# Performance work log

Hardware: AMD Instinct MI355X
Metric: run time of the kernel (lower is better)

The kernel has to match this reference:

```python
import jax, jax.numpy as jnp
import numpy as np

N_NODES = 500000
N_EDGES = 4000000
IN_DIM = 2
HID = 8
N_ITERS = 3


def _edge_net(x, row, col, e1_w, e1_b, e2_w, e2_b):
    # bi = x[col], bo = x[row]; B = cat([bi, bo]) is detached in torch
    B = jax.lax.stop_gradient(jnp.concatenate([x[col], x[row]], axis=-1))  # [E, 2*F]
    h = jnp.tanh(B @ e1_w + e1_b)
    return jax.nn.sigmoid(h @ e2_w + e2_b)  # [E, 1]


def _node_net(x, row, col, edge_attr, n1_w, n1_b, n2_w, n2_b):
    e = jax.lax.stop_gradient(edge_attr)  # [E, 1], detached in torch
    bi = x[col] * e  # [E, F]
    bo = x[row] * e
    mi = jax.ops.segment_sum(bo, col, num_segments=N_NODES)  # scatter_add over col
    mo = jax.ops.segment_sum(bi, row, num_segments=N_NODES)  # scatter_add over row
    M = jax.lax.stop_gradient(jnp.concatenate([mi, mo, x], axis=-1))  # [N, 3*F]
    h = jnp.tanh(M @ n1_w + n1_b)
    return jnp.tanh(h @ n2_w + n2_b)  # [N, HID]


def setup_inputs() -> dict:
    key = jax.random.key(0)
    ks = jax.random.split(key, 12)
    F = IN_DIM + HID  # 10
    s = lambda fan_in: 1.0 / np.sqrt(fan_in)
    return {
        "x": jax.random.normal(ks[0], (N_NODES, IN_DIM), jnp.float32),
        "edge_index": jax.random.randint(ks[1], (2, N_EDGES), 0, N_NODES),
        "win_w": jax.random.uniform(ks[2], (IN_DIM, HID), jnp.float32, -s(IN_DIM), s(IN_DIM)),
        "win_b": jax.random.uniform(ks[3], (HID,), jnp.float32, -s(IN_DIM), s(IN_DIM)),
        "e1_w": jax.random.uniform(ks[4], (2 * F, HID), jnp.float32, -s(2 * F), s(2 * F)),
        "e1_b": jax.random.uniform(ks[5], (HID,), jnp.float32, -s(2 * F), s(2 * F)),
        "e2_w": jax.random.uniform(ks[6], (HID, 1), jnp.float32, -s(HID), s(HID)),
        "e2_b": jax.random.uniform(ks[7], (1,), jnp.float32, -s(HID), s(HID)),
        "n1_w": jax.random.uniform(ks[8], (3 * F, HID), jnp.float32, -s(3 * F), s(3 * F)),
        "n1_b": jax.random.uniform(ks[9], (HID,), jnp.float32, -s(3 * F), s(3 * F)),
        "n2_w": jax.random.uniform(ks[10], (HID, HID), jnp.float32, -s(HID), s(HID)),
        "n2_b": jax.random.uniform(ks[11], (HID,), jnp.float32, -s(HID), s(HID)),
    }


def reference(x, edge_index, win_w, win_b, e1_w, e1_b, e2_w, e2_b, n1_w, n1_b, n2_w, n2_b):
    row, col = edge_index[0], edge_index[1]
    X = x
    H = jnp.tanh(X @ win_w + win_b)  # input_network
    xcat = jnp.concatenate([H, X], axis=-1)  # [N, 10]
    for _ in range(N_ITERS):
        e = _edge_net(xcat, row, col, e1_w, e1_b, e2_w, e2_b)
        H = _node_net(xcat, row, col, e, n1_w, n1_b, n2_w, n2_b)
        xcat = jnp.concatenate([H, X], axis=-1)
    out = _edge_net(xcat, row, col, e1_w, e1_b, e2_w, e2_b)
    return out.squeeze(-1)  # [E]
```

## Files before the change

### kernel.cpp

```cpp
#include <hip/hip_runtime.h>
#include <hip/hip_fp16.h>
#include <math.h>

#define N_NODES 500000
#define N_EDGES 4000000
#define FDIM 10
#define HID 8

#define DSPACE (2 * N_NODES)
#define NB 512
#define BSHIFT 11
#define BMASK 2047
#define NB_USED ((DSPACE + BMASK) / 2048)

#define IN_BLOCKS ((N_NODES + 255) / 256)
#define ROWS_PAD (IN_BLOCKS * 256)
#define NODE_BLOCKS2 ((N_NODES + 127) / 128)

__device__ __forceinline__ float fast_tanh(float x) {
    float e = __builtin_amdgcn_exp2f(x * 2.885390082f);
    return 1.0f - 2.0f * __builtin_amdgcn_rcpf(e + 1.0f);
}
__device__ __forceinline__ float fast_sigmoid(float x) {
    float e = __builtin_amdgcn_exp2f(-1.442695041f * x);
    return __builtin_amdgcn_rcpf(1.0f + e);
}

__device__ __forceinline__ float2 h2f2(float bits) {
    union { float f; __half2 h; } u; u.f = bits;
    return __half22float2(u.h);
}
__device__ __forceinline__ float f2h2(float a, float b) {
    union { float f; __half2 h; } u; u.h = __floats2half2_rn(a, b);
    return u.f;
}

__device__ __forceinline__ void unpack10(float4 H, float X, float* o) {
    float2 p0 = h2f2(H.x), p1 = h2f2(H.y), p2 = h2f2(H.z), p3 = h2f2(H.w), p4 = h2f2(X);
    o[0] = p0.x; o[1] = p0.y; o[2] = p1.x; o[3] = p1.y; o[4] = p2.x;
    o[5] = p2.y; o[6] = p3.x; o[7] = p3.y; o[8] = p4.x; o[9] = p4.y;
}

__device__ __forceinline__ void fma8(float* a, float xk, float4 wa, float4 wb) {
    a[0] += xk * wa.x; a[1] += xk * wa.y; a[2] += xk * wa.z; a[3] += xk * wa.w;
    a[4] += xk * wb.x; a[5] += xk * wb.y; a[6] += xk * wb.z; a[7] += xk * wb.w;
}

__global__ __launch_bounds__(256) void input_kernel(const float* __restrict__ x,
                                                    const float* __restrict__ win_w,
                                                    const float* __restrict__ win_b,
                                                    float4* __restrict__ xh,
                                                    float* __restrict__ xs) {
    int n = blockIdx.x * 256 + threadIdx.x;
    float x0 = 0.f, x1 = 0.f;
    if (n < N_NODES) { x0 = x[2 * n]; x1 = x[2 * n + 1]; }
    float h[HID];
#pragma unroll
    for (int j = 0; j < HID; j++)
        h[j] = fast_tanh(x0 * win_w[j] + x1 * win_w[HID + j] + win_b[j]);
    xh[n] = make_float4(f2h2(h[0], h[1]), f2h2(h[2], h[3]),
                        f2h2(h[4], h[5]), f2h2(h[6], h[7]));
    xs[n] = f2h2(x0, x1);
}

__global__ void bucket_hist_kernel(const int* __restrict__ row,
                                   const int* __restrict__ col,
                                   int* __restrict__ g_cnt) {
    __shared__ int s_cnt[NB];
    int tid = threadIdx.x;
    for (int i = tid; i < NB; i += 256) s_cnt[i] = 0;
    __syncthreads();
    int base = blockIdx.x * 4096;
#pragma unroll
    for (int k = 0; k < 16; k++) {
        int e = base + k * 256 + tid;
        if (e < N_EDGES) {
            int c = col[e], r = row[e];
            atomicAdd(&s_cnt[(2 * c) >> BSHIFT], 1);
            atomicAdd(&s_cnt[(2 * r + 1) >> BSHIFT], 1);
        }
    }
    __syncthreads();
    for (int i = tid; i < NB; i += 256) {
        int v = s_cnt[i];
        if (v) atomicAdd(&g_cnt[i], v);
    }
}

__global__ void bucket_scan_kernel(const int* __restrict__ g_cnt,
                                   int* __restrict__ bucket_base,
                                   int* __restrict__ bucket_cur) {
    __shared__ int s[NB];
    int t = threadIdx.x;
    int c = g_cnt[t];
    s[t] = c;
    __syncthreads();
    for (int off = 1; off < NB; off <<= 1) {
        int v = (t >= off) ? s[t - off] : 0;
        __syncthreads();
        s[t] += v;
        __syncthreads();
    }
    int ex = s[t] - c;
    bucket_base[t] = ex;
    bucket_cur[t] = ex;
    if (t == NB - 1) bucket_base[NB] = s[t];
}

__global__ void bin_kernel(const int* __restrict__ row,
                           const int* __restrict__ col,
                           int* __restrict__ bucket_cur,
                           unsigned int* __restrict__ binned) {
    __shared__ int s_cnt[NB];
    __shared__ int s_start[NB];
    __shared__ int s_cur[NB];
    __shared__ int s_gbase[NB];
    __shared__ unsigned int s_items[8192];
    __shared__ unsigned short s_ibkt[8192];

    int tid = threadIdx.x;
    if (tid < NB) s_cnt[tid] = 0;
    __syncthreads();

    int base = blockIdx.x * 4096;
    int cc[4], rr[4];
#pragma unroll
    for (int k = 0; k < 4; k++) {
        int e = base + k * 1024 + tid;
        bool ok = (e < N_EDGES);
        cc[k] = ok ? col[e] : -1;
        rr[k] = ok ? row[e] : -1;
        if (ok) {
            atomicAdd(&s_cnt[(2 * cc[k]) >> BSHIFT], 1);
            atomicAdd(&s_cnt[(2 * rr[k] + 1) >> BSHIFT], 1);
        }
    }
    __syncthreads();

    if (tid < NB) s_start[tid] = s_cnt[tid];
    __syncthreads();
    for (int off = 1; off < NB; off <<= 1) {
        int v = 0;
        if (tid < NB && tid >= off) v = s_start[tid - off];
        __syncthreads();
        if (tid < NB) s_start[tid] += v;
        __syncthreads();
    }
    if (tid < NB) {
        int ex = s_start[tid] - s_cnt[tid];
        s_start[tid] = ex;
        s_cur[tid] = ex;
    }
    __syncthreads();

#pragma unroll
    for (int k = 0; k < 4; k++) {
        if (cc[k] >= 0) {
            int d0 = 2 * cc[k];
            int b0 = d0 >> BSHIFT;
            int s0 = atomicAdd(&s_cur[b0], 1);
            s_items[s0] = ((unsigned)(d0 & BMASK) << 19) | (unsigned)rr[k];
            s_ibkt[s0] = (unsigned short)b0;
            int d1 = 2 * rr[k] + 1;
            int b1 = d1 >> BSHIFT;
            int s1 = atomicAdd(&s_cur[b1], 1);
            s_items[s1] = ((unsigned)(d1 & BMASK) << 19) | (unsigned)cc[k];
            s_ibkt[s1] = (unsigned short)b1;
        }
    }
    __syncthreads();

    if (tid < NB) s_gbase[tid] = atomicAdd(&bucket_cur[tid], s_cnt[tid]);
    __syncthreads();

    int tot = s_start[NB - 1] + s_cnt[NB - 1];
    for (int s = tid; s < tot; s += 1024) {
        int b = s_ibkt[s];
        int g = s_gbase[b] + (s - s_start[b]);
        binned[g] = s_items[s];
    }
}

__global__ void csr_kernel(const unsigned int* __restrict__ binned,
                           const int* __restrict__ bucket_base,
                           int* __restrict__ offs,
                           int* __restrict__ entries) {
    __shared__ int s_deg[2048];
    __shared__ int s_cur[2048];
    __shared__ int s_pair[1024];

    int t = threadIdx.x;
    int b = blockIdx.x;
    if (b == 0 && t == 0) offs[DSPACE] = 2 * N_EDGES;

    int ebase = bucket_base[b];
    int eend = bucket_base[b + 1];

    s_deg[t] = 0;
    s_deg[t + 1024] = 0;
    __syncthreads();

    for (int p = ebase + t; p < eend; p += 1024)
        atomicAdd(&s_deg[binned[p] >> 19], 1);
    __syncthreads();

    int d0 = s_deg[2 * t], d1 = s_deg[2 * t + 1];
    s_pair[t] = d0 + d1;
    __syncthreads();
    for (int off = 1; off < 1024; off <<= 1) {
        int v = (t >= off) ? s_pair[t - off] : 0;
        __syncthreads();
        s_pair[t] += v;
        __syncthreads();
    }
    int pex = s_pair[t] - (d0 + d1);
    s_cur[2 * t] = pex;
    s_cur[2 * t + 1] = pex + d0;

    int dest0 = b * 2048 + 2 * t;
    if (dest0 < DSPACE) offs[dest0] = ebase + pex;
    if (dest0 + 1 < DSPACE) offs[dest0 + 1] = ebase + pex + d0;
    __syncthreads();

    for (int p = ebase + t; p < eend; p += 1024) {
        unsigned int it = binned[p];
        int dl = it >> 19;
        int other = it & 0x7FFFF;
        int pos = atomicAdd(&s_cur[dl], 1);
        entries[ebase + pos] = other;
    }
}

__global__ __launch_bounds__(256) void edge_kernel(const int* __restrict__ row,
                                                   const int* __restrict__ col,
                                                   const float4* __restrict__ xh,
                                                   const float* __restrict__ xs,
                                                   const float* __restrict__ e1_w,
                                                   const float* __restrict__ e1_b,
                                                   const float* __restrict__ e2_w,
                                                   const float* __restrict__ e2_b,
                                                   float* __restrict__ out) {
    __shared__ float4 s_w4[40];
    __shared__ float s_b[HID];
    __shared__ float s_v[HID];
    __shared__ float s_c[1];
    int tid = threadIdx.x;
    float* wf = (float*)s_w4;
    if (tid < 160) wf[tid] = e1_w[tid];
    else if (tid < 168) s_b[tid - 160] = e1_b[tid - 160];
    else if (tid < 176) s_v[tid - 168] = e2_w[tid - 168];
    else if (tid == 176) s_c[0] = e2_b[0];
    __syncthreads();

    int i = blockIdx.x * 256 + tid;
    if (i >= N_EDGES) return;

    int r = row[i], c = col[i];
    float4 aH = xh[c]; float aX = xs[c];
    float4 bH = xh[r]; float bX = xs[r];
    float a[FDIM], bb[FDIM];
    unpack10(aH, aX, a);
    unpack10(bH, bX, bb);

    float acc[HID];
#pragma unroll
    for (int j = 0; j < HID; j++) acc[j] = s_b[j];
#pragma unroll
    for (int k = 0; k < FDIM; k++)
        fma8(acc, a[k], s_w4[2 * k], s_w4[2 * k + 1]);
#pragma unroll
    for (int k = 0; k < FDIM; k++)
        fma8(acc, bb[k], s_w4[20 + 2 * k], s_w4[21 + 2 * k]);

    float d = s_c[0];
#pragma unroll
    for (int j = 0; j < HID; j++) d += fast_tanh(acc[j]) * s_v[j];
    out[i] = fast_sigmoid(d);
}

__global__ __launch_bounds__(256) void node_kernel(const float4* __restrict__ xh,
                                                   const float* __restrict__ xs,
                                                   const int* __restrict__ offs,
                                                   const int* __restrict__ entries,
                                                   const float* __restrict__ e1_w,
                                                   const float* __restrict__ e1_b,
                                                   const float* __restrict__ e2_w,
                                                   const float* __restrict__ e2_b,
                                                   const float* __restrict__ n1_w,
                                                   const float* __restrict__ n1_b,
                                                   const float* __restrict__ n2_w,
                                                   const float* __restrict__ n2_b,
                                                   float4* __restrict__ xh_next) {
    __shared__ float4 s_e1w4[40];
    __shared__ float s_e1b[HID];
    __shared__ float s_e2w[HID];
    __shared__ float s_e2b[1];
    __shared__ float4 s_n1w4[60];
    __shared__ float s_n1b[HID];
    __shared__ float4 s_n2w4[16];
    __shared__ float s_n2b[HID];
    __shared__ float s_mo[128 * 11];

    int tid = threadIdx.x;
    float* e1f = (float*)s_e1w4;
    if (tid < 160) e1f[tid] = e1_w[tid];
    else if (tid < 168) s_e1b[tid - 160] = e1_b[tid - 160];
    else if (tid < 176) s_e2w[tid - 168] = e2_w[tid - 168];
    else if (tid == 176) s_e2b[0] = e2_b[0];
    float* n1f = (float*)s_n1w4;
    if (tid < 240) n1f[tid] = n1_w[tid];
    else if (tid < 248) s_n1b[tid - 240] = n1_b[tid - 240];
    float* n2f = (float*)s_n2w4;
    if (tid < 64) n2f[tid] = n2_w[tid];
    else if (tid < 72) s_n2b[tid - 64] = n2_b[tid - 64];
    __syncthreads();

    bool up = tid >= 128;
    int lt = up ? tid - 128 : tid;
    int n = blockIdx.x * 128 + lt;
    bool act = n < N_NODES;

    int selfBase = up ? 20 : 0;
    int othBase  = up ? 0 : 20;
    int dest = 2 * n + (up ? 1 : 0);

    float e2w_r[HID];
#pragma unroll
    for (int j = 0; j < HID; j++) e2w_r[j] = s_e2w[j];
    float e2b_r = s_e2b[0];

    float xn[FDIM];
    float m[FDIM];
#pragma unroll
    for (int k = 0; k < FDIM; k++) m[k] = 0.f;

    if (act) {
        float4 hN = xh[n]; float xN = xs[n];
        unpack10(hN, xN, xn);

        float us[HID];
#pragma unroll
        for (int j = 0; j < HID; j++) us[j] = s_e1b[j];
#pragma unroll
        for (int k = 0; k < FDIM; k++)
            fma8(us, xn[k], s_e1w4[selfBase + 2 * k], s_e1w4[selfBase + 2 * k + 1]);

        int p0 = offs[dest], p1 = offs[dest + 1];
        float4 cH = make_float4(0.f, 0.f, 0.f, 0.f); float cX = 0.f;
        if (p0 < p1) { int o = entries[p0]; cH = xh[o]; cX = xs[o]; }
        for (int p = p0; p < p1; ++p) {
            float4 nH = cH; float nX = cX;
            if (p + 1 < p1) { int o2 = entries[p + 1]; nH = xh[o2]; nX = xs[o2]; }

            float xo[FDIM];
            unpack10(cH, cX, xo);

            float acc[HID];
#pragma unroll
            for (int j = 0; j < HID; j++) acc[j] = us[j];
#pragma unroll
            for (int k = 0; k < FDIM; k++)
                fma8(acc, xo[k], s_e1w4[othBase + 2 * k], s_e1w4[othBase + 2 * k + 1]);

            float d = e2b_r;
#pragma unroll
            for (int j = 0; j < HID; j++) d += fast_tanh(acc[j]) * e2w_r[j];
            float e = fast_sigmoid(d);
#pragma unroll
            for (int k = 0; k < FDIM; k++) m[k] += e * xo[k];

            cH = nH; cX = nX;
        }
    }

    if (up && act) {
        int lb = lt * 11;
#pragma unroll
        for (int k = 0; k < FDIM; k++) s_mo[lb + k] = m[k];
    }
    __syncthreads();

    if (!up && act) {
        int lb = lt * 11;
        float h1[HID];
#pragma unroll
        for (int j = 0; j < HID; j++) h1[j] = s_n1b[j];
#pragma unroll
        for (int k = 0; k < FDIM; k++)
            fma8(h1, m[k], s_n1w4[2 * k], s_n1w4[2 * k + 1]);
#pragma unroll
        for (int k = 0; k < FDIM; k++)
            fma8(h1, s_mo[lb + k], s_n1w4[20 + 2 * k], s_n1w4[21 + 2 * k]);
#pragma unroll
        for (int k = 0; k < FDIM; k++)
            fma8(h1, xn[k], s_n1w4[40 + 2 * k], s_n1w4[41 + 2 * k]);
#pragma unroll
        for (int j = 0; j < HID; j++) h1[j] = fast_tanh(h1[j]);

        float H[HID];
#pragma unroll
        for (int j = 0; j < HID; j++) H[j] = s_n2b[j];
#pragma unroll
        for (int k = 0; k < HID; k++)
            fma8(H, h1[k], s_n2w4[2 * k], s_n2w4[2 * k + 1]);
#pragma unroll
        for (int j = 0; j < HID; j++) H[j] = fast_tanh(H[j]);

        xh_next[n] = make_float4(f2h2(H[0], H[1]), f2h2(H[2], H[3]),
                                 f2h2(H[4], H[5]), f2h2(H[6], H[7]));
    }
}

extern "C" void kernel_launch(void* const* d_in, const int* in_sizes, int n_in,
                              void* d_out, int out_size, void* d_ws, size_t ws_size,
                              hipStream_t stream) {
    const float* x      = (const float*)d_in[0];
    const int*   eidx   = (const int*)d_in[1];
    const float* win_w  = (const float*)d_in[2];
    const float* win_b  = (const float*)d_in[3];
    const float* e1_w   = (const float*)d_in[4];
    const float* e1_b   = (const float*)d_in[5];
    const float* e2_w   = (const float*)d_in[6];
    const float* e2_b   = (const float*)d_in[7];
    const float* n1_w   = (const float*)d_in[8];
    const float* n1_b   = (const float*)d_in[9];
    const float* n2_w   = (const float*)d_in[10];
    const float* n2_b   = (const float*)d_in[11];
    float* out = (float*)d_out;

    const int* row = eidx;
    const int* col = eidx + N_EDGES;

    float4* xh0 = (float4*)d_ws;
    float4* xh1 = xh0 + ROWS_PAD;
    float*  xs  = (float*)(xh1 + ROWS_PAD);
    unsigned int* binned = (unsigned int*)(xs + ROWS_PAD);
    int* entries = (int*)(binned + 2 * (size_t)N_EDGES);
    int* offs        = entries + 2 * (size_t)N_EDGES;
    int* g_cnt       = offs + DSPACE + 64;
    int* bucket_base = g_cnt + NB;
    int* bucket_cur  = bucket_base + NB + 64;

    const int BLK = 256;
    int edge_blocks = (N_EDGES + BLK - 1) / BLK;
    int chunk_blocks = (N_EDGES + 4095) / 4096;

    hipMemsetAsync(g_cnt, 0, NB * sizeof(int), stream);
    bucket_hist_kernel<<<chunk_blocks, 256, 0, stream>>>(row, col, g_cnt);
    bucket_scan_kernel<<<1, NB, 0, stream>>>(g_cnt, bucket_base, bucket_cur);
    bin_kernel<<<chunk_blocks, 1024, 0, stream>>>(row, col, bucket_cur, binned);
    csr_kernel<<<NB_USED, 1024, 0, stream>>>(binned, bucket_base, offs, entries);

    input_kernel<<<IN_BLOCKS, BLK, 0, stream>>>(x, win_w, win_b, xh0, xs);

    float4* cur = xh0;
    float4* nxt = xh1;
    for (int it = 0; it < 3; it++) {
        node_kernel<<<NODE_BLOCKS2, BLK, 0, stream>>>(
            cur, xs, offs, entries, e1_w, e1_b, e2_w, e2_b,
            n1_w, n1_b, n2_w, n2_b, nxt);
        float4* t = cur; cur = nxt; nxt = t;
    }

    edge_kernel<<<edge_blocks, BLK, 0, stream>>>(
        row, col, cur, xs, e1_w, e1_b, e2_w, e2_b, out);
}
```

Baseline: 930.9 us.

## Split node kernel into per-side gather and node-net kernels using fp16 dot2

```diff
diff --git a/kernel.cpp b/kernel.cpp
--- a/kernel.cpp
+++ b/kernel.cpp
@@ -15,7 +15,22 @@
 
 #define IN_BLOCKS ((N_NODES + 255) / 256)
 #define ROWS_PAD (IN_BLOCKS * 256)
-#define NODE_BLOCKS2 ((N_NODES + 127) / 128)
+#define MSTRIDE ((size_t)ROWS_PAD * 10)
+
+typedef _Float16 h2v __attribute__((ext_vector_type(2)));
+
+__device__ __forceinline__ h2v u2h(unsigned x) {
+    union { unsigned u; h2v h; } t; t.u = x; return t.h;
+}
+__device__ __forceinline__ unsigned packh2(float a, float b) {
+    union { __half2 h; unsigned u; } t; t.h = __floats2half2_rn(a, b); return t.u;
+}
+__device__ __forceinline__ float rfl_f(float x) {
+    return __int_as_float(__builtin_amdgcn_readfirstlane(__float_as_int(x)));
+}
+__device__ __forceinline__ unsigned rfl_u(unsigned x) {
+    return (unsigned)__builtin_amdgcn_readfirstlane((int)x);
+}
 
 __device__ __forceinline__ float fast_tanh(float x) {
     float e = __builtin_amdgcn_exp2f(x * 2.885390082f);
@@ -26,31 +41,11 @@
     return __builtin_amdgcn_rcpf(1.0f + e);
 }
 
-__device__ __forceinline__ float2 h2f2(float bits) {
-    union { float f; __half2 h; } u; u.f = bits;
-    return __half22float2(u.h);
-}
-__device__ __forceinline__ float f2h2(float a, float b) {
-    union { float f; __half2 h; } u; u.h = __floats2half2_rn(a, b);
-    return u.f;
-}
-
-__device__ __forceinline__ void unpack10(float4 H, float X, float* o) {
-    float2 p0 = h2f2(H.x), p1 = h2f2(H.y), p2 = h2f2(H.z), p3 = h2f2(H.w), p4 = h2f2(X);
-    o[0] = p0.x; o[1] = p0.y; o[2] = p1.x; o[3] = p1.y; o[4] = p2.x;
-    o[5] = p2.y; o[6] = p3.x; o[7] = p3.y; o[8] = p4.x; o[9] = p4.y;
-}
-
-__device__ __forceinline__ void fma8(float* a, float xk, float4 wa, float4 wb) {
-    a[0] += xk * wa.x; a[1] += xk * wa.y; a[2] += xk * wa.z; a[3] += xk * wa.w;
-    a[4] += xk * wb.x; a[5] += xk * wb.y; a[6] += xk * wb.z; a[7] += xk * wb.w;
-}
-
 __global__ __launch_bounds__(256) void input_kernel(const float* __restrict__ x,
                                                     const float* __restrict__ win_w,
                                                     const float* __restrict__ win_b,
-                                                    float4* __restrict__ xh,
-                                                    float* __restrict__ xs) {
+                                                    uint4* __restrict__ xh,
+                                                    unsigned* __restrict__ xs) {
     int n = blockIdx.x * 256 + threadIdx.x;
     float x0 = 0.f, x1 = 0.f;
     if (n < N_NODES) { x0 = x[2 * n]; x1 = x[2 * n + 1]; }
@@ -58,9 +53,9 @@
 #pragma unroll
     for (int j = 0; j < HID; j++)
         h[j] = fast_tanh(x0 * win_w[j] + x1 * win_w[HID + j] + win_b[j]);
-    xh[n] = make_float4(f2h2(h[0], h[1]), f2h2(h[2], h[3]),
-                        f2h2(h[4], h[5]), f2h2(h[6], h[7]));
-    xs[n] = f2h2(x0, x1);
+    xh[n] = make_uint4(packh2(h[0], h[1]), packh2(h[2], h[3]),
+                       packh2(h[4], h[5]), packh2(h[6], h[7]));
+    xs[n] = packh2(x0, x1);
 }
 
 __global__ void bucket_hist_kernel(const int* __restrict__ row,
@@ -231,184 +226,251 @@
     }
 }
 
+__global__ __launch_bounds__(256, 6) void node_loop_kernel(
+        const uint4* __restrict__ xh,
+        const unsigned* __restrict__ xs,
+        const int* __restrict__ offs,
+        const int* __restrict__ entries,
+        const float* __restrict__ e1_w,
+        const float* __restrict__ e1_b,
+        const float* __restrict__ e2_w,
+        const float* __restrict__ e2_b,
+        float* __restrict__ m_out) {
+    __shared__ uint4 s_self4[10];
+    __shared__ unsigned s_oth[40];
+    __shared__ float s_scal[17];
+
+    int tid = threadIdx.x;
+    int side = (blockIdx.x >= IN_BLOCKS) ? 1 : 0;
+    int selfBase = side ? 10 : 0;
+    int othBase  = side ? 0 : 10;
+
+    unsigned* s_self = (unsigned*)s_self4;
+    if (tid < 40) {
+        int kk = tid >> 3, j = tid & 7;
+        s_self[tid] = packh2(e1_w[(selfBase + 2 * kk) * HID + j],
+                             e1_w[(selfBase + 2 * kk + 1) * HID + j]);
+        s_oth[tid]  = packh2(e1_w[(othBase + 2 * kk) * HID + j],
+                             e1_w[(othBase + 2 * kk + 1) * HID + j]);
+    } else if (tid < 48) s_scal[tid - 40] = e1_b[tid - 48 + 8];
+    else if (tid < 56) s_scal[tid - 40] = e2_w[tid - 48];
+    else if (tid == 56) s_scal[16] = e2_b[0];
+    __syncthreads();
+
+    unsigned so[40];
+#pragma unroll
+    for (int i = 0; i < 40; i++) so[i] = rfl_u(s_oth[i]);
+    float sb[HID], sv[HID];
+#pragma unroll
+    for (int j = 0; j < HID; j++) { sb[j] = rfl_f(s_scal[j]); sv[j] = rfl_f(s_scal[8 + j]); }
+    float sc = rfl_f(s_scal[16]);
+
+    int n = (blockIdx.x - side * IN_BLOCKS) * 256 + tid;
+    if (n >= N_NODES) return;
+    int dest = 2 * n + side;
+
+    uint4 xq = xh[n]; unsigned xx = xs[n];
+    unsigned xp[5] = { xq.x, xq.y, xq.z, xq.w, xx };
+    float us[HID];
+#pragma unroll
+    for (int j = 0; j < HID; j++) us[j] = sb[j];
+#pragma unroll
+    for (int kk = 0; kk < 5; kk++) {
+        uint4 wa = s_self4[2 * kk];
+        uint4 wb = s_self4[2 * kk + 1];
+        h2v a = u2h(xp[kk]);
+        us[0] = __builtin_amdgcn_fdot2(a, u2h(wa.x), us[0], false);
+        us[1] = __builtin_amdgcn_fdot2(a, u2h(wa.y), us[1], false);
+        us[2] = __builtin_amdgcn_fdot2(a, u2h(wa.z), us[2], false);
+        us[3] = __builtin_amdgcn_fdot2(a, u2h(wa.w), us[3], false);
+        us[4] = __builtin_amdgcn_fdot2(a, u2h(wb.x), us[4], false);
+        us[5] = __builtin_amdgcn_fdot2(a, u2h(wb.y), us[5], false);
+        us[6] = __builtin_amdgcn_fdot2(a, u2h(wb.z), us[6], false);
+        us[7] = __builtin_amdgcn_fdot2(a, u2h(wb.w), us[7], false);
+    }
+
+    int p0 = offs[dest], p1 = offs[dest + 1];
+    float m[FDIM];
+#pragma unroll
+    for (int k = 0; k < FDIM; k++) m[k] = 0.f;
+
+    uint4 cH = make_uint4(0, 0, 0, 0); unsigned cX = 0;
+    if (p0 < p1) { int o = entries[p0]; cH = xh[o]; cX = xs[o]; }
+    for (int p = p0; p < p1; ++p) {
+        uint4 nH = cH; unsigned nX = cX;
+        if (p + 1 < p1) { int o2 = entries[p + 1]; nH = xh[o2]; nX = xs[o2]; }
+
+        unsigned cp[5] = { cH.x, cH.y, cH.z, cH.w, cX };
+        float acc[HID];
+#pragma unroll
+        for (int j = 0; j < HID; j++) acc[j] = us[j];
+#pragma unroll
+        for (int kk = 0; kk < 5; kk++) {
+            h2v a = u2h(cp[kk]);
+#pragma unroll
+            for (int j = 0; j < HID; j++)
+                acc[j] = __builtin_amdgcn_fdot2(a, u2h(so[kk * 8 + j]), acc[j], false);
+        }
+        float d = sc;
+#pragma unroll
+        for (int j = 0; j < HID; j++) d += fast_tanh(acc[j]) * sv[j];
+        float e = fast_sigmoid(d);
+#pragma unroll
+        for (int kk = 0; kk < 5; kk++) {
+            h2v a = u2h(cp[kk]);
+            m[2 * kk]     += e * (float)a.x;
+            m[2 * kk + 1] += e * (float)a.y;
+        }
+        cH = nH; cX = nX;
+    }
+
+    float2* md = (float2*)(m_out + (size_t)side * MSTRIDE + (size_t)n * 10);
+    md[0] = make_float2(m[0], m[1]);
+    md[1] = make_float2(m[2], m[3]);
+    md[2] = make_float2(m[4], m[5]);
+    md[3] = make_float2(m[6], m[7]);
+    md[4] = make_float2(m[8], m[9]);
+}
+
+__global__ __launch_bounds__(256) void node_net_kernel(
+        const uint4* __restrict__ xh,
+        const unsigned* __restrict__ xs,
+        const float* __restrict__ m_in,
+        const float* __restrict__ n1_w,
+        const float* __restrict__ n1_b,
+        const float* __restrict__ n2_w,
+        const float* __restrict__ n2_b,
+        uint4* __restrict__ xh_next) {
+    __shared__ float s_n1w[30 * HID];
+    __shared__ float s_n1b[HID];
+    __shared__ float s_n2w[HID * HID];
+    __shared__ float s_n2b[HID];
+    int tid = threadIdx.x;
+    if (tid < 240) s_n1w[tid] = n1_w[tid];
+    else if (tid < 248) s_n1b[tid - 240] = n1_b[tid - 240];
+    if (tid < 64) s_n2w[tid] = n2_w[tid];
+    else if (tid < 72) s_n2b[tid - 64] = n2_b[tid - 64];
+    __syncthreads();
+
+    int n = blockIdx.x * 256 + tid;
+    if (n >= N_NODES) return;
+
+    float mi[FDIM], mo[FDIM];
+    const float2* p_mi = (const float2*)(m_in + (size_t)n * 10);
+    const float2* p_mo = (const float2*)(m_in + MSTRIDE + (size_t)n * 10);
+#pragma unroll
+    for (int k = 0; k < 5; k++) {
+        float2 a = p_mi[k]; mi[2 * k] = a.x; mi[2 * k + 1] = a.y;
+        float2 b = p_mo[k]; mo[2 * k] = b.x; mo[2 * k + 1] = b.y;
+    }
+    uint4 xq = xh[n]; unsigned xx = xs[n];
+    unsigned xp[5] = { xq.x, xq.y, xq.z, xq.w, xx };
+    float xn[FDIM];
+#pragma unroll
+    for (int kk = 0; kk < 5; kk++) {
+        h2v a = u2h(xp[kk]);
+        xn[2 * kk] = (float)a.x; xn[2 * kk + 1] = (float)a.y;
+    }
+
+    float h1[HID];
+#pragma unroll
+    for (int j = 0; j < HID; j++) h1[j] = s_n1b[j];
+#pragma unroll
+    for (int k = 0; k < FDIM; k++) {
+#pragma unroll
+        for (int j = 0; j < HID; j++) {
+            h1[j] += mi[k] * s_n1w[k * HID + j];
+            h1[j] += mo[k] * s_n1w[(FDIM + k) * HID + j];
+            h1[j] += xn[k] * s_n1w[(2 * FDIM + k) * HID + j];
+        }
+    }
+#pragma unroll
+    for (int j = 0; j < HID; j++) h1[j] = fast_tanh(h1[j]);
+
+    float H[HID];
+#pragma unroll
+    for (int j = 0; j < HID; j++) H[j] = s_n2b[j];
+#pragma unroll
+    for (int k = 0; k < HID; k++) {
+#pragma unroll
+        for (int j = 0; j < HID; j++) H[j] += h1[k] * s_n2w[k * HID + j];
+    }
+#pragma unroll
+    for (int j = 0; j < HID; j++) H[j] = fast_tanh(H[j]);
+
+    xh_next[n] = make_uint4(packh2(H[0], H[1]), packh2(H[2], H[3]),
+                            packh2(H[4], H[5]), packh2(H[6], H[7]));
+}
+
 __global__ __launch_bounds__(256) void edge_kernel(const int* __restrict__ row,
                                                    const int* __restrict__ col,
-                                                   const float4* __restrict__ xh,
-                                                   const float* __restrict__ xs,
+                                                   const uint4* __restrict__ xh,
+                                                   const unsigned* __restrict__ xs,
                                                    const float* __restrict__ e1_w,
                                                    const float* __restrict__ e1_b,
                                                    const float* __restrict__ e2_w,
                                                    const float* __restrict__ e2_b,
                                                    float* __restrict__ out) {
-    __shared__ float4 s_w4[40];
-    __shared__ float s_b[HID];
-    __shared__ float s_v[HID];
-    __shared__ float s_c[1];
+    __shared__ unsigned s_top[40];
+    __shared__ uint4 s_bot4[10];
+    __shared__ float s_scal[17];
     int tid = threadIdx.x;
-    float* wf = (float*)s_w4;
-    if (tid < 160) wf[tid] = e1_w[tid];
-    else if (tid < 168) s_b[tid - 160] = e1_b[tid - 160];
-    else if (tid < 176) s_v[tid - 168] = e2_w[tid - 168];
-    else if (tid == 176) s_c[0] = e2_b[0];
-    __syncthreads();
+    unsigned* s_bot = (unsigned*)s_bot4;
+    if (tid < 40) {
+        int kk = tid >> 3, j = tid & 7;
+        s_top[tid] = packh2(e1_w[(2 * kk) * HID + j], e1_w[(2 * kk + 1) * HID + j]);
+        s_bot[tid] = packh2(e1_w[(FDIM + 2 * kk) * HID + j], e1_w[(FDIM + 2 * kk + 1) * HID + j]);
+    } else if (tid < 48) s_scal[tid - 40] = e1_b[tid - 48 + 8];
+    else if (tid < 56) s_scal[tid - 40] = e2_w[tid - 48];
+    else if (tid == 56) s_scal[16] = e2_b[0];
+    __syncthreads();
+
+    unsigned st[40];
+#pragma unroll
+    for (int i = 0; i < 40; i++) st[i] = rfl_u(s_top[i]);
+    float sb[HID], sv[HID];
+#pragma unroll
+    for (int j = 0; j < HID; j++) { sb[j] = rfl_f(s_scal[j]); sv[j] = rfl_f(s_scal[8 + j]); }
+    float sc = rfl_f(s_scal[16]);
 
     int i = blockIdx.x * 256 + tid;
     if (i >= N_EDGES) return;
 
     int r = row[i], c = col[i];
-    float4 aH = xh[c]; float aX = xs[c];
-    float4 bH = xh[r]; float bX = xs[r];
-    float a[FDIM], bb[FDIM];
-    unpack10(aH, aX, a);
-    unpack10(bH, bX, bb);
+    uint4 aq = xh[c]; unsigned ax = xs[c];
+    uint4 bq = xh[r]; unsigned bx = xs[r];
+    unsigned ap[5] = { aq.x, aq.y, aq.z, aq.w, ax };
+    unsigned bp[5] = { bq.x, bq.y, bq.z, bq.w, bx };
 
     float acc[HID];
 #pragma unroll
-    for (int j = 0; j < HID; j++) acc[j] = s_b[j];
-#pragma unroll
-    for (int k = 0; k < FDIM; k++)
-        fma8(acc, a[k], s_w4[2 * k], s_w4[2 * k + 1]);
-#pragma unroll
-    for (int k = 0; k < FDIM; k++)
-        fma8(acc, bb[k], s_w4[20 + 2 * k], s_w4[21 + 2 * k]);
-
-    float d = s_c[0];
-#pragma unroll
-    for (int j = 0; j < HID; j++) d += fast_tanh(acc[j]) * s_v[j];
+    for (int j = 0; j < HID; j++) acc[j] = sb[j];
+#pragma unroll
+    for (int kk = 0; kk < 5; kk++) {
+        h2v a = u2h(ap[kk]);
+#pragma unroll
+        for (int j = 0; j < HID; j++)
+            acc[j] = __builtin_amdgcn_fdot2(a, u2h(st[kk * 8 + j]), acc[j], false);
+    }
+#pragma unroll
+    for (int kk = 0; kk < 5; kk++) {
+        uint4 wa = s_bot4[2 * kk];
+        uint4 wb = s_bot4[2 * kk + 1];
+        h2v b = u2h(bp[kk]);
+        acc[0] = __builtin_amdgcn_fdot2(b, u2h(wa.x), acc[0], false);
+        acc[1] = __builtin_amdgcn_fdot2(b, u2h(wa.y), acc[1], false);
+        acc[2] = __builtin_amdgcn_fdot2(b, u2h(wa.z), acc[2], false);
+        acc[3] = __builtin_amdgcn_fdot2(b, u2h(wa.w), acc[3], false);
+        acc[4] = __builtin_amdgcn_fdot2(b, u2h(wb.x), acc[4], false);
+        acc[5] = __builtin_amdgcn_fdot2(b, u2h(wb.y), acc[5], false);
+        acc[6] = __builtin_amdgcn_fdot2(b, u2h(wb.z), acc[6], false);
+        acc[7] = __builtin_amdgcn_fdot2(b, u2h(wb.w), acc[7], false);
+    }
+
+    float d = sc;
+#pragma unroll
+    for (int j = 0; j < HID; j++) d += fast_tanh(acc[j]) * sv[j];
     out[i] = fast_sigmoid(d);
-}
-
-__global__ __launch_bounds__(256) void node_kernel(const float4* __restrict__ xh,
-                                                   const float* __restrict__ xs,
-                                                   const int* __restrict__ offs,
-                                                   const int* __restrict__ entries,
-                                                   const float* __restrict__ e1_w,
-                                                   const float* __restrict__ e1_b,
-                                                   const float* __restrict__ e2_w,
-                                                   const float* __restrict__ e2_b,
-                                                   const float* __restrict__ n1_w,
-                                                   const float* __restrict__ n1_b,
-                                                   const float* __restrict__ n2_w,
-                                                   const float* __restrict__ n2_b,
-                                                   float4* __restrict__ xh_next) {
-    __shared__ float4 s_e1w4[40];
-    __shared__ float s_e1b[HID];
-    __shared__ float s_e2w[HID];
-    __shared__ float s_e2b[1];
-    __shared__ float4 s_n1w4[60];
-    __shared__ float s_n1b[HID];
-    __shared__ float4 s_n2w4[16];
-    __shared__ float s_n2b[HID];
-    __shared__ float s_mo[128 * 11];
-
-    int tid = threadIdx.x;
-    float* e1f = (float*)s_e1w4;
-    if (tid < 160) e1f[tid] = e1_w[tid];
-    else if (tid < 168) s_e1b[tid - 160] = e1_b[tid - 160];
-    else if (tid < 176) s_e2w[tid - 168] = e2_w[tid - 168];
-    else if (tid == 176) s_e2b[0] = e2_b[0];
-    float* n1f = (float*)s_n1w4;
-    if (tid < 240) n1f[tid] = n1_w[tid];
-    else if (tid < 248) s_n1b[tid - 240] = n1_b[tid - 240];
-    float* n2f = (float*)s_n2w4;
-    if (tid < 64) n2f[tid] = n2_w[tid];
-    else if (tid < 72) s_n2b[tid - 64] = n2_b[tid - 64];
-    __syncthreads();
-
-    bool up = tid >= 128;
-    int lt = up ? tid - 128 : tid;
-    int n = blockIdx.x * 128 + lt;
-    bool act = n < N_NODES;
-
-    int selfBase = up ? 20 : 0;
-    int othBase  = up ? 0 : 20;
-    int dest = 2 * n + (up ? 1 : 0);
-
-    float e2w_r[HID];
-#pragma unroll
-    for (int j = 0; j < HID; j++) e2w_r[j] = s_e2w[j];
-    float e2b_r = s_e2b[0];
-
-    float xn[FDIM];
-    float m[FDIM];
-#pragma unroll
-    for (int k = 0; k < FDIM; k++) m[k] = 0.f;
-
-    if (act) {
-        float4 hN = xh[n]; float xN = xs[n];
-        unpack10(hN, xN, xn);
-
-        float us[HID];
-#pragma unroll
-        for (int j = 0; j < HID; j++) us[j] = s_e1b[j];
-#pragma unroll
-        for (int k = 0; k < FDIM; k++)
-            fma8(us, xn[k], s_e1w4[selfBase + 2 * k], s_e1w4[selfBase + 2 * k + 1]);
-
-        int p0 = offs[dest], p1 = offs[dest + 1];
-        float4 cH = make_float4(0.f, 0.f, 0.f, 0.f); float cX = 0.f;
-        if (p0 < p1) { int o = entries[p0]; cH = xh[o]; cX = xs[o]; }
-        for (int p = p0; p < p1; ++p) {
-            float4 nH = cH; float nX = cX;
-            if (p + 1 < p1) { int o2 = entries[p + 1]; nH = xh[o2]; nX = xs[o2]; }
-
-            float xo[FDIM];
-            unpack10(cH, cX, xo);
-
-            float acc[HID];
-#pragma unroll
-            for (int j = 0; j < HID; j++) acc[j] = us[j];
-#pragma unroll
-            for (int k = 0; k < FDIM; k++)
-                fma8(acc, xo[k], s_e1w4[othBase + 2 * k], s_e1w4[othBase + 2 * k + 1]);
-
-            float d = e2b_r;
-#pragma unroll
-            for (int j = 0; j < HID; j++) d += fast_tanh(acc[j]) * e2w_r[j];
-            float e = fast_sigmoid(d);
-#pragma unroll
-            for (int k = 0; k < FDIM; k++) m[k] += e * xo[k];
-
-            cH = nH; cX = nX;
-        }
-    }
-
-    if (up && act) {
-        int lb = lt * 11;
-#pragma unroll
-        for (int k = 0; k < FDIM; k++) s_mo[lb + k] = m[k];
-    }
-    __syncthreads();
-
-    if (!up && act) {
-        int lb = lt * 11;
-        float h1[HID];
-#pragma unroll
-        for (int j = 0; j < HID; j++) h1[j] = s_n1b[j];
-#pragma unroll
-        for (int k = 0; k < FDIM; k++)
-            fma8(h1, m[k], s_n1w4[2 * k], s_n1w4[2 * k + 1]);
-#pragma unroll
-        for (int k = 0; k < FDIM; k++)
-            fma8(h1, s_mo[lb + k], s_n1w4[20 + 2 * k], s_n1w4[21 + 2 * k]);
-#pragma unroll
-        for (int k = 0; k < FDIM; k++)
-            fma8(h1, xn[k], s_n1w4[40 + 2 * k], s_n1w4[41 + 2 * k]);
-#pragma unroll
-        for (int j = 0; j < HID; j++) h1[j] = fast_tanh(h1[j]);
-
-        float H[HID];
-#pragma unroll
-        for (int j = 0; j < HID; j++) H[j] = s_n2b[j];
-#pragma unroll
-        for (int k = 0; k < HID; k++)
-            fma8(H, h1[k], s_n2w4[2 * k], s_n2w4[2 * k + 1]);
-#pragma unroll
-        for (int j = 0; j < HID; j++) H[j] = fast_tanh(H[j]);
-
-        xh_next[n] = make_float4(f2h2(H[0], H[1]), f2h2(H[2], H[3]),
-                                 f2h2(H[4], H[5]), f2h2(H[6], H[7]));
-    }
 }
 
 extern "C" void kernel_launch(void* const* d_in, const int* in_sizes, int n_in,
@@ -431,15 +493,18 @@
     const int* row = eidx;
     const int* col = eidx + N_EDGES;
 
-    float4* xh0 = (float4*)d_ws;
-    float4* xh1 = xh0 + ROWS_PAD;
-    float*  xs  = (float*)(xh1 + ROWS_PAD);
-    unsigned int* binned = (unsigned int*)(xs + ROWS_PAD);
-    int* entries = (int*)(binned + 2 * (size_t)N_EDGES);
-    int* offs        = entries + 2 * (size_t)N_EDGES;
-    int* g_cnt       = offs + DSPACE + 64;
-    int* bucket_base = g_cnt + NB;
-    int* bucket_cur  = bucket_base + NB + 64;
+    char* w = (char*)d_ws;
+    uint4* xh0 = (uint4*)w;            w += (size_t)ROWS_PAD * 16;
+    uint4* xh1 = (uint4*)w;            w += (size_t)ROWS_PAD * 16;
+    unsigned* xs = (unsigned*)w;       w += (size_t)ROWS_PAD * 4;
+    int* entries = (int*)w;            w += (size_t)2 * N_EDGES * 4;
+    int* offs = (int*)w;               w += (size_t)(DSPACE + 64) * 4;
+    int* g_cnt = (int*)w;              w += NB * 4;
+    int* bucket_base = (int*)w;        w += (NB + 64) * 4;
+    int* bucket_cur = (int*)w;         w += NB * 4;
+    w = (char*)(((uintptr_t)w + 255) & ~(uintptr_t)255);
+    float* m = (float*)w;
+    unsigned int* binned = (unsigned int*)w;
 
     const int BLK = 256;
     int edge_blocks = (N_EDGES + BLK - 1) / BLK;
@@ -453,13 +518,14 @@
 
     input_kernel<<<IN_BLOCKS, BLK, 0, stream>>>(x, win_w, win_b, xh0, xs);
 
-    float4* cur = xh0;
-    float4* nxt = xh1;
+    uint4* cur = xh0;
+    uint4* nxt = xh1;
     for (int it = 0; it < 3; it++) {
-        node_kernel<<<NODE_BLOCKS2, BLK, 0, stream>>>(
-            cur, xs, offs, entries, e1_w, e1_b, e2_w, e2_b,
-            n1_w, n1_b, n2_w, n2_b, nxt);
-        float4* t = cur; cur = nxt; nxt = t;
+        node_loop_kernel<<<2 * IN_BLOCKS, BLK, 0, stream>>>(
+            cur, xs, offs, entries, e1_w, e1_b, e2_w, e2_b, m);
+        node_net_kernel<<<IN_BLOCKS, BLK, 0, stream>>>(
+            cur, xs, m, n1_w, n1_b, n2_w, n2_b, nxt);
+        uint4* t = cur; cur = nxt; nxt = t;
     }
 
     edge_kernel<<<edge_blocks, BLK, 0, stream>>>(
```

Result: slower. 1.183 ms (+27.1%).
